# Kernel optimization log

Measured on AMD Instinct MI355X. Metric: run time of the kernel, lower is better.

## Reference

```python
import jax, jax.numpy as jnp
import numpy as np

DIM = 1024
HEADS = 16
HEAD_DIM = DIM // HEADS
D_FF = 4 * DIM
EPS = 1e-5


def _layernorm(x, g, b):
    mu = jnp.mean(x, axis=-1, keepdims=True)
    var = jnp.mean(jnp.square(x - mu), axis=-1, keepdims=True)
    return (x - mu) * jax.lax.rsqrt(var + EPS) * g + b


def setup_inputs() -> dict:
    key = jax.random.key(0)
    ks = jax.random.split(key, 8)
    s = 0.02
    return {
        "x": jax.random.normal(ks[0], (2, 2048, DIM), dtype=jnp.float32),
        "Wqkv": jax.random.normal(ks[1], (DIM, 3 * DIM), dtype=jnp.float32) * s,
        "bqkv": jnp.zeros((3 * DIM,), dtype=jnp.float32),
        "Wout": jax.random.normal(ks[2], (DIM, DIM), dtype=jnp.float32) * s,
        "bout": jnp.zeros((DIM,), dtype=jnp.float32),
        "W1": jax.random.normal(ks[3], (DIM, D_FF), dtype=jnp.float32) * s,
        "b1": jnp.zeros((D_FF,), dtype=jnp.float32),
        "W2": jax.random.normal(ks[4], (D_FF, DIM), dtype=jnp.float32) * s,
        "b2": jnp.zeros((DIM,), dtype=jnp.float32),
        "g1": jnp.ones((DIM,), dtype=jnp.float32),
        "be1": jnp.zeros((DIM,), dtype=jnp.float32),
        "g2": jnp.ones((DIM,), dtype=jnp.float32),
        "be2": jnp.zeros((DIM,), dtype=jnp.float32),
    }


def reference(x, Wqkv, bqkv, Wout, bout, W1, b1, W2, b2, g1, be1, g2, be2):
    B, T, C = x.shape
    # --- multi-head self-attention (explicit QK^T softmax, no mask/cache) ---
    qkv = (x @ Wqkv + bqkv).reshape(B, T, 3, HEADS, HEAD_DIM)
    q = qkv[:, :, 0].transpose(0, 2, 1, 3)  # (B,H,T,hd)
    k = qkv[:, :, 1].transpose(0, 2, 1, 3)
    v = qkv[:, :, 2].transpose(0, 2, 1, 3)
    scale = HEAD_DIM ** -0.5
    scores = jnp.einsum("bhqd,bhkd->bhqk", q, k) * scale  # (B,H,T,T)
    attn = jax.nn.softmax(scores, axis=-1)
    o = jnp.einsum("bhqk,bhkd->bhqd", attn, v)
    o = o.transpose(0, 2, 1, 3).reshape(B, T, C)
    attn_out = o @ Wout + bout
    # --- Post-LN: LN applied to sublayer output, then residual ---
    x = x + _layernorm(attn_out, g1, be1)
    # --- FFN with exact GELU ---
    h = jax.nn.gelu(x @ W1 + b1, approximate=False)
    ffn_out = h @ W2 + b2
    x = x + _layernorm(ffn_out, g2, be2)
    return x
```

## Files before the change

### kernel.cpp

```cpp
#include <hip/hip_runtime.h>
#include <cstdint>
#include <cstddef>

#define DIM 1024
#define HEADS 16
#define HD 64
#define DFF 4096
#define TSEQ 2048
#define EPS 1e-5f

#define WAITCNT_VM4 0xF74
#define WAITCNT_VM0 0xF70
#define WAITCNT_VM8 0xF78
#define WAITCNT_LGKM0 0xC07F

typedef __bf16 bf16x8 __attribute__((ext_vector_type(8)));
typedef __bf16 bf16x4 __attribute__((ext_vector_type(4)));
typedef float floatx4 __attribute__((ext_vector_type(4)));

__device__ __forceinline__ unsigned short f2bf(float f) {
  union { float f; unsigned int u; } v; v.f = f;
  return (unsigned short)((v.u + 0x7FFFu + ((v.u >> 16) & 1u)) >> 16);
}

__device__ __forceinline__ float exp2_fast(float x) {
#if __has_builtin(__builtin_amdgcn_exp2f)
  return __builtin_amdgcn_exp2f(x);
#else
  float r;
  asm("v_exp_f32 %0, %1" : "=v"(r) : "v"(x));
  return r;
#endif
}

__device__ __forceinline__ float gelu_f(float v) {
  const float u = v * (0.7978845608f + 0.0356774081f * v * v);
  const float e = __expf(2.0f * u);
  const float t = 1.0f - 2.0f / (e + 1.0f);
  return 0.5f * v * (1.0f + t);
}

__device__ __forceinline__ void async16(const void* g, void* l) {
  __builtin_amdgcn_global_load_lds(
      (const __attribute__((address_space(1))) void*)g,
      (__attribute__((address_space(3))) void*)l, 16, 0, 0);
}

__global__ __launch_bounds__(256) void prep_all(const float* __restrict__ x,
                                                const float* __restrict__ Wqkv,
                                                const float* __restrict__ Wout,
                                                const float* __restrict__ W1,
                                                const float* __restrict__ W2,
                                                unsigned short* __restrict__ xb,
                                                unsigned short* __restrict__ WqkvT,
                                                unsigned short* __restrict__ WoutT,
                                                unsigned short* __restrict__ W1T,
                                                unsigned short* __restrict__ W2T) {
  const int bid = blockIdx.x;
  const int tid = threadIdx.x;
  if (bid < 4096) {
    const int i = bid * 256 + tid;
    float4 v = ((const float4*)x)[i];
    ushort4 o;
    o.x = f2bf(v.x); o.y = f2bf(v.y); o.z = f2bf(v.z); o.w = f2bf(v.w);
    ((ushort4*)xb)[i] = o;
    return;
  }
  int id = bid - 4096;
  const float* src; unsigned short* dst; int R, C, gx;
  if (id < 3072)      {            src = Wqkv; dst = WqkvT; R = 1024; C = 3072; gx = 96; }
  else if (id < 4096) { id -= 3072; src = Wout; dst = WoutT; R = 1024; C = 1024; gx = 32; }
  else if (id < 8192) { id -= 4096; src = W1;   dst = W1T;   R = 1024; C = 4096; gx = 128; }
  else                { id -= 8192; src = W2;   dst = W2T;   R = 4096; C = 1024; gx = 32; }
  const int c0 = (id % gx) * 32, r0 = (id / gx) * 32;
  const int tx = tid & 31, ty = tid >> 5;
  __shared__ float tile[32][33];
#pragma unroll
  for (int i = 0; i < 32; i += 8)
    tile[ty + i][tx] = src[(size_t)(r0 + ty + i) * C + c0 + tx];
  __syncthreads();
#pragma unroll
  for (int i = 0; i < 32; i += 8)
    dst[(size_t)(c0 + ty + i) * R + r0 + tx] = f2bf(tile[tx][ty + i]);
}

#define GEMM256_CORE(APTR, BPTR, KT, KOFF, NG_)                                       \
  const int lane = tid & 63, wv = tid >> 6;                                           \
  const int l16 = lane & 15, quad = lane >> 4;                                        \
  const int wr = wv >> 2, wc = wv & 3;                                                \
  const int srow = tid >> 3;                                                          \
  const int scc = (tid & 7) ^ (srow & 7);                                             \
  const unsigned short* Asrc = (APTR) + (size_t)(bm + srow) * (KT) + (KOFF) + scc * 8;\
  const unsigned short* Bsrc = (BPTR) + (size_t)(bn + srow) * (KT) + (KOFF) + scc * 8;\
  auto stageKstep = [&](int buf, int kk) {                                            \
    char* dA = smem + buf * 65536;                                                    \
    char* dB = dA + 32768;                                                            \
    _Pragma("unroll")                                                                 \
    for (int h = 0; h < 2; h++)                                                       \
      _Pragma("unroll")                                                               \
      for (int j = 0; j < 2; j++) {                                                   \
        async16(Asrc + (size_t)(h * 128 + 64 * j) * (KT) + kk,                        \
                dA + h * 16384 + (j * 512 + tid) * 16);                               \
        async16(Bsrc + (size_t)(h * 128 + 64 * j) * (KT) + kk,                        \
                dB + h * 16384 + (j * 512 + tid) * 16);                               \
      }                                                                               \
  };                                                                                  \
  floatx4 acc[8][4] = {};                                                             \
  stageKstep(0, 0);                                                                   \
  __builtin_amdgcn_s_waitcnt(WAITCNT_VM0);                                            \
  __builtin_amdgcn_s_barrier();                                                       \
  for (int g = 0; g < (NG_); g++) {                                                   \
    const int p = g & 1;                                                              \
    const char* Ab = smem + p * 65536 + wr * 16384;                                   \
    const char* Bb = smem + p * 65536 + 32768 + (wc >> 1) * 16384;                    \
    bf16x8 bg[4][2];                                                                  \
    _Pragma("unroll")                                                                 \
    for (int q = 0; q < 4; q++) {                                                     \
      if (q == 0) {                                                                   \
        if (g + 1 < (NG_)) stageKstep(p ^ 1, (g + 1) << 6);                           \
        _Pragma("unroll")                                                             \
        for (int ni = 0; ni < 4; ni++) {                                              \
          const int lr = (wc & 1) * 64 + ni * 16 + l16;                               \
          _Pragma("unroll")                                                           \
          for (int ks = 0; ks < 2; ks++)                                              \
            bg[ni][ks] = *(const bf16x8*)(Bb + lr * 128 +                             \
                                          (((quad + 4 * ks) ^ (lr & 7)) * 16));       \
        }                                                                             \
      }                                                                               \
      bf16x8 af[2][2];                                                                \
      _Pragma("unroll")                                                               \
      for (int m = 0; m < 2; m++) {                                                   \
        const int lr = (q * 2 + m) * 16 + l16;                                        \
        _Pragma("unroll")                                                             \
        for (int ks = 0; ks < 2; ks++)                                                \
          af[m][ks] = *(const bf16x8*)(Ab + lr * 128 +                                \
                                       (((quad + 4 * ks) ^ (lr & 7)) * 16));          \
      }                                                                               \
      __builtin_amdgcn_s_barrier();                                                   \
      __builtin_amdgcn_s_waitcnt(WAITCNT_LGKM0);                                      \
      __builtin_amdgcn_s_setprio(1);                                                  \
      _Pragma("unroll")                                                               \
      for (int ks = 0; ks < 2; ks++)                                                  \
        _Pragma("unroll")                                                             \
        for (int ni = 0; ni < 4; ni++)                                                \
          _Pragma("unroll")                                                           \
          for (int m = 0; m < 2; m++)                                                 \
            acc[q * 2 + m][ni] = __builtin_amdgcn_mfma_f32_16x16x32_bf16(             \
                af[m][ks], bg[ni][ks], acc[q * 2 + m][ni], 0, 0, 0);                  \
      __builtin_amdgcn_s_setprio(0);                                                  \
      if (q == 3) __builtin_amdgcn_s_waitcnt(WAITCNT_VM0);                            \
      __builtin_amdgcn_s_barrier();                                                   \
    }                                                                                 \
  }

__global__ __launch_bounds__(512, 2) void gemm256g(const unsigned short* __restrict__ A,
                                                   const unsigned short* __restrict__ Bt,
                                                   const float* __restrict__ bias,
                                                   unsigned short* __restrict__ Cout,
                                                   int M, int N, int K) {
  extern __shared__ char smem[];
  const int tid = threadIdx.x;
  int bxx = blockIdx.x, byy = blockIdx.y;
  {
    const int id = byy * 16 + bxx;
    const int xcd = id & 7, sub = id >> 3;
    bxx = (xcd & 3) * 4 + (sub & 3);
    byy = (xcd >> 2) * 8 + (sub >> 2);
  }
  const int bm = byy * 256, bn = bxx * 256;
  GEMM256_CORE(A, Bt, K, 0, K >> 6)

  __syncthreads();
  unsigned short* eb = (unsigned short*)smem + wv * 1152;
  float bvv[4];
#pragma unroll
  for (int ni = 0; ni < 4; ni++) bvv[ni] = bias[bn + wc * 64 + ni * 16 + l16];
  const int lrow = lane >> 2, ck = lane & 3;
#pragma unroll
  for (int mi = 0; mi < 8; mi++) {
#pragma unroll
    for (int ni = 0; ni < 4; ni++)
#pragma unroll
      for (int r = 0; r < 4; r++)
        eb[(quad * 4 + r) * 72 + ni * 16 + l16] =
            f2bf(gelu_f(acc[mi][ni][r] + bvv[ni]));
    __syncthreads();
    unsigned short* gp =
        Cout + (size_t)(bm + wr * 128 + mi * 16 + lrow) * N + bn + wc * 64;
#pragma unroll
    for (int j = 0; j < 2; j++)
      *(uint4*)(gp + j * 32 + ck * 8) = *(const uint4*)&eb[lrow * 72 + j * 32 + ck * 8];
    __syncthreads();
  }
}

__global__ __launch_bounds__(512, 2) void gemm256_qkv(const unsigned short* __restrict__ A,
                                                      const unsigned short* __restrict__ Bt,
                                                      const float* __restrict__ bias,
                                                      unsigned short* __restrict__ Qg,
                                                      unsigned short* __restrict__ Kg,
                                                      unsigned short* __restrict__ Vtg) {
  extern __shared__ char smem[];
  const int tid = threadIdx.x;
  const int id = blockIdx.y * 12 + blockIdx.x;
  const int xcd = id / 24, sub = id % 24;
  const int bxx = (xcd & 3) * 3 + sub % 3;
  const int byy = (xcd >> 2) * 8 + sub / 3;
  const int bm = byy * 256, bn = bxx * 256;
  GEMM256_CORE(A, Bt, 1024, 0, 16)

  const float QSCALE = 0.125f * 1.44269504089f;
#pragma unroll
  for (int ni = 0; ni < 4; ni++) {
    const int col = bn + wc * 64 + ni * 16 + l16;
    const float bv = bias[col];
    const int sec = col >> 10;
    const int cc = col & 1023;
    const int hh = cc >> 6, dd = cc & 63;
#pragma unroll
    for (int mi = 0; mi < 8; mi++) {
      const int row0 = bm + wr * 128 + mi * 16 + quad * 4;
      const int b2 = row0 >> 11, tt0 = row0 & 2047;
      if (sec == 0) {
        unsigned short* q = Qg + ((size_t)(b2 * HEADS + hh) * TSEQ + tt0) * HD + dd;
#pragma unroll
        for (int r = 0; r < 4; r++)
          q[(size_t)r * HD] = f2bf((acc[mi][ni][r] + bv) * QSCALE);
      } else if (sec == 1) {
        unsigned short* k = Kg + ((size_t)(b2 * HEADS + hh) * TSEQ + tt0) * HD + dd;
#pragma unroll
        for (int r = 0; r < 4; r++)
          k[(size_t)r * HD] = f2bf(acc[mi][ni][r] + bv);
      } else {
        ushort4 o;
        o.x = f2bf(acc[mi][ni][0] + bv);
        o.y = f2bf(acc[mi][ni][1] + bv);
        o.z = f2bf(acc[mi][ni][2] + bv);
        o.w = f2bf(acc[mi][ni][3] + bv);
        *(ushort4*)(Vtg + ((size_t)(b2 * HEADS + hh) * HD + dd) * TSEQ + tt0) = o;
      }
    }
  }
}

__global__ __launch_bounds__(512, 2) void gemm256_sk(const unsigned short* __restrict__ A,
                                                     const unsigned short* __restrict__ Bt,
                                                     float* __restrict__ Cp,
                                                     int M, int N, int Ktot, int Ksl) {
  extern __shared__ char smem[];
  const int tid = threadIdx.x;
  const int id = (blockIdx.z * 16 + blockIdx.y) * 4 + blockIdx.x;
  const int xcd = id >> 5, sub = id & 31;
  const int bxx = sub & 3;
  const int u = xcd * 8 + (sub >> 2);
  const int byy = u & 15, bz = u >> 4;
  const int bm = byy * 256, bn = bxx * 256;
  const int koff = bz * Ksl;
  GEMM256_CORE(A, Bt, Ktot, koff, Ksl >> 6)

  float* out = Cp + (size_t)bz * M * (size_t)N;
#pragma unroll
  for (int ni = 0; ni < 4; ni++) {
    const int col = bn + wc * 64 + ni * 16 + l16;
#pragma unroll
    for (int mi = 0; mi < 8; mi++) {
      const int row0 = bm + wr * 128 + mi * 16 + quad * 4;
#pragma unroll
      for (int r = 0; r < 4; r++)
        out[(size_t)(row0 + r) * N + col] = acc[mi][ni][r];
    }
  }
}

__global__ __launch_bounds__(256, 4) void attn_mfma(const unsigned short* __restrict__ Qg,
                                                    const unsigned short* __restrict__ Kg,
                                                    const unsigned short* __restrict__ Vtg,
                                                    unsigned short* __restrict__ ob) {
  __shared__ __align__(16) char smem[40960];
  unsigned short* QPs = (unsigned short*)smem;

  const int bid = blockIdx.x;
  const int lid = (bid & 7) * 128 + (bid >> 3);
  const int qt = lid & 31;
  const int h = (lid >> 5) & 15;
  const int b = lid >> 9;
  const int tid = threadIdx.x;
  const int w = tid >> 6, lane = tid & 63, l16 = lane & 15, quad = lane >> 4;
  const int qg = w >> 1;
  const int kh = w & 1;

  const int r0 = tid >> 3;
  const int c0 = (tid & 7) ^ (r0 & 7);

  const char* Qbase = (const char*)(Qg + ((size_t)(b * HEADS + h) * TSEQ + qt * 64) * HD);
  const char* Kbase = (const char*)(Kg + (size_t)(b * HEADS + h) * TSEQ * HD);
  const char* Vbase = (const char*)(Vtg + (size_t)(b * HEADS + h) * HD * TSEQ);

  auto Ksp = [&](int s) -> char* { return smem + 8192 + s * 8192; };
  auto Vsp = [&](int s) -> char* { return smem + 24576 + s * 8192; };

  auto issueKV = [&](int s, int ch) {
    const size_t koff = (size_t)ch * 64;
#pragma unroll
    for (int i = 0; i < 2; i++) {
      async16(Kbase + (koff + r0 + i * 32) * 128 + c0 * 16, Ksp(s) + (i * 256 + tid) * 16);
      async16(Vbase + (size_t)(r0 + i * 32) * (TSEQ * 2) + koff * 2 + c0 * 16,
              Vsp(s) + (i * 256 + tid) * 16);
    }
  };

#pragma unroll
  for (int i = 0; i < 2; i++)
    async16(Qbase + (size_t)(r0 + i * 32) * 128 + c0 * 16, (char*)QPs + (i * 256 + tid) * 16);
  issueKV(0, 0);
  issueKV(1, 1);

  __builtin_amdgcn_s_waitcnt(WAITCNT_VM8);
  __builtin_amdgcn_s_barrier();

  bf16x8 qf[2][2];
#pragma unroll
  for (int mi = 0; mi < 2; mi++)
#pragma unroll
    for (int kt = 0; kt < 2; kt++) {
      const int row = qg * 32 + mi * 16 + l16;
      qf[mi][kt] = *(const bf16x8*)((const char*)QPs + row * 128 +
                                    (((quad + 4 * kt) ^ (row & 7)) * 16));
    }
  __builtin_amdgcn_s_waitcnt(WAITCNT_LGKM0);
  __builtin_amdgcn_sched_barrier(0);

  union { unsigned short u[8]; bf16x8 b; } onesu;
#pragma unroll
  for (int j = 0; j < 8; j++) onesu.u[j] = 0x3F80;
  const bf16x8 ones = onesu.b;

  floatx4 oacc[2][5] = {};
  char* Pw = (char*)QPs + w * 1152;

  const int NC = TSEQ / 64;
  int sidx = 0;
  for (int ch = 0; ch < NC; ch++) {
    if (ch < NC - 1) __builtin_amdgcn_s_waitcnt(WAITCNT_VM4);
    else             __builtin_amdgcn_s_waitcnt(WAITCNT_VM0);
    __builtin_amdgcn_s_barrier();

    floatx4 sacc[2][2] = {};
    __builtin_amdgcn_s_setprio(1);
#pragma unroll
    for (int kt = 0; kt < 2; kt++) {
#pragma unroll
      for (int ni = 0; ni < 2; ni++) {
        const int krow = kh * 32 + ni * 16 + l16;
        bf16x8 kf = *(const bf16x8*)(Ksp(sidx) + krow * 128 +
                                     (((quad + 4 * kt) ^ (krow & 7)) * 16));
#pragma unroll
        for (int mi = 0; mi < 2; mi++)
          sacc[mi][ni] =
              __builtin_amdgcn_mfma_f32_16x16x32_bf16(qf[mi][kt], kf, sacc[mi][ni], 0, 0, 0);
      }
    }
    __builtin_amdgcn_s_setprio(0);

    bf16x8 pf[2];
#pragma unroll
    for (int mi = 0; mi < 2; mi++) {
#pragma unroll
      for (int ni = 0; ni < 2; ni++)
#pragma unroll
        for (int r = 0; r < 4; r++) {
          const float p = exp2_fast(sacc[mi][ni][r]);
          const unsigned int pu = __builtin_bit_cast(unsigned int, p);
          *((unsigned short*)(Pw + (quad * 4 + r) * 72 + (ni * 16 + l16) * 2)) =
              (unsigned short)(pu >> 16);
        }
      union { bf16x8 v8; bf16x4 v4[2]; } u;
      u.v4[0] = *(const bf16x4*)(Pw + l16 * 72 + quad * 16);
      u.v4[1] = *(const bf16x4*)(Pw + l16 * 72 + quad * 16 + 8);
      pf[mi] = u.v8;
    }

    __builtin_amdgcn_s_setprio(1);
#pragma unroll
    for (int nj = 0; nj < 4; nj++) {
      const int vrow = nj * 16 + l16;
      bf16x8 vf = *(const bf16x8*)(Vsp(sidx) + vrow * 128 +
                                   (((quad + 4 * kh) ^ (vrow & 7)) * 16));
#pragma unroll
      for (int mi = 0; mi < 2; mi++)
        oacc[mi][nj] = __builtin_amdgcn_mfma_f32_16x16x32_bf16(pf[mi], vf, oacc[mi][nj], 0, 0, 0);
    }
#pragma unroll
    for (int mi = 0; mi < 2; mi++)
      oacc[mi][4] = __builtin_amdgcn_mfma_f32_16x16x32_bf16(pf[mi], ones, oacc[mi][4], 0, 0, 0);
    __builtin_amdgcn_s_setprio(0);

    __builtin_amdgcn_s_waitcnt(WAITCNT_LGKM0);
    __builtin_amdgcn_s_barrier();
    if (ch + 2 < NC) issueKV(sidx, ch + 2);
    sidx ^= 1;
  }

  __syncthreads();
  float* Op = (float*)smem + qg * (32 * 66);
  if (kh == 1) {
#pragma unroll
    for (int mi = 0; mi < 2; mi++)
#pragma unroll
      for (int r = 0; r < 4; r++) {
        const int row = mi * 16 + quad * 4 + r;
#pragma unroll
        for (int nj = 0; nj < 4; nj++)
          Op[row * 66 + nj * 16 + l16] = oacc[mi][nj][r];
        if (l16 == 0) Op[row * 66 + 64] = oacc[mi][4][r];
      }
  }
  __syncthreads();
  if (kh == 0) {
#pragma unroll
    for (int mi = 0; mi < 2; mi++)
#pragma unroll
      for (int r = 0; r < 4; r++) {
        const int row = mi * 16 + quad * 4 + r;
        const float inv = 1.0f / (oacc[mi][4][r] + Op[row * 66 + 64]);
        const int t = qt * 64 + qg * 32 + row;
        unsigned short* orow = ob + (size_t)(b * TSEQ + t) * DIM + h * HD + l16;
#pragma unroll
        for (int nj = 0; nj < 4; nj++)
          orow[nj * 16] = f2bf((oacc[mi][nj][r] + Op[row * 66 + nj * 16 + l16]) * inv);
      }
  }
}

template <int NP, int WBF>
__global__ __launch_bounds__(256) void add_ln_red(const float* __restrict__ xin,
                                                  const float* __restrict__ parts,
                                                  const float* __restrict__ bias,
                                                  const float* __restrict__ gw,
                                                  const float* __restrict__ bw,
                                                  float* __restrict__ xout,
                                                  unsigned short* __restrict__ xbf) {
  const size_t MN = (size_t)4096 * DIM;
  const int row = blockIdx.x;
  const int tid = threadIdx.x;
  const int c = tid * 4;
  const size_t base = (size_t)row * DIM;
  float4 v = *(const float4*)(parts + base + c);
#pragma unroll
  for (int p = 1; p < NP; p++) {
    float4 t = *(const float4*)(parts + p * MN + base + c);
    v.x += t.x; v.y += t.y; v.z += t.z; v.w += t.w;
  }
  float4 bb = *(const float4*)(bias + c);
  v.x += bb.x; v.y += bb.y; v.z += bb.z; v.w += bb.w;

  float s = v.x + v.y + v.z + v.w;
  float s2 = v.x * v.x + v.y * v.y + v.z * v.z + v.w * v.w;
#pragma unroll
  for (int off = 1; off < 64; off <<= 1) {
    s += __shfl_xor(s, off);
    s2 += __shfl_xor(s2, off);
  }
  __shared__ float rsum[4], rsq[4];
  if ((tid & 63) == 0) { rsum[tid >> 6] = s; rsq[tid >> 6] = s2; }
  __syncthreads();
  s = rsum[0] + rsum[1] + rsum[2] + rsum[3];
  s2 = rsq[0] + rsq[1] + rsq[2] + rsq[3];
  const float mu = s * (1.0f / DIM);
  const float var = s2 * (1.0f / DIM) - mu * mu;
  const float rstd = rsqrtf(var + EPS);
  float4 xv = *(const float4*)(xin + base + c);
  float4 gv = *(const float4*)(gw + c);
  float4 bv = *(const float4*)(bw + c);
  float4 o;
  o.x = xv.x + (v.x - mu) * rstd * gv.x + bv.x;
  o.y = xv.y + (v.y - mu) * rstd * gv.y + bv.y;
  o.z = xv.z + (v.z - mu) * rstd * gv.z + bv.z;
  o.w = xv.w + (v.w - mu) * rstd * gv.w + bv.w;
  *(float4*)(xout + base + c) = o;
  if (WBF) {
    ushort4 ob;
    ob.x = f2bf(o.x); ob.y = f2bf(o.y); ob.z = f2bf(o.z); ob.w = f2bf(o.w);
    *(ushort4*)(xbf + base + c) = ob;
  }
}

extern "C" void kernel_launch(void* const* d_in, const int* in_sizes, int n_in,
                              void* d_out, int out_size, void* d_ws, size_t ws_size,
                              hipStream_t stream) {
  const float* x    = (const float*)d_in[0];
  const float* Wqkv = (const float*)d_in[1];
  const float* bqkv = (const float*)d_in[2];
  const float* Wout = (const float*)d_in[3];
  const float* bout = (const float*)d_in[4];
  const float* W1   = (const float*)d_in[5];
  const float* b1   = (const float*)d_in[6];
  const float* W2   = (const float*)d_in[7];
  const float* b2   = (const float*)d_in[8];
  const float* g1   = (const float*)d_in[9];
  const float* be1  = (const float*)d_in[10];
  const float* g2   = (const float*)d_in[11];
  const float* be2  = (const float*)d_in[12];

  static bool s_attr = false;
  if (!s_attr) {
    hipFuncSetAttribute((const void*)gemm256g,
                        hipFuncAttributeMaxDynamicSharedMemorySize, 131072);
    hipFuncSetAttribute((const void*)gemm256_qkv,
                        hipFuncAttributeMaxDynamicSharedMemorySize, 131072);
    hipFuncSetAttribute((const void*)gemm256_sk,
                        hipFuncAttributeMaxDynamicSharedMemorySize, 131072);
    s_attr = true;
  }

  char* w = (char*)d_ws;
  const size_t MB = 1048576;
  unsigned short* xb     = (unsigned short*)(w + 0 * MB);
  unsigned short* WqkvT  = (unsigned short*)(w + 8 * MB);
  unsigned short* WoutT  = (unsigned short*)(w + 14 * MB);
  unsigned short* W1T    = (unsigned short*)(w + 16 * MB);
  unsigned short* W2T    = (unsigned short*)(w + 24 * MB);
  unsigned short* Qb     = (unsigned short*)(w + 32 * MB);
  unsigned short* Kb     = (unsigned short*)(w + 40 * MB);
  unsigned short* Vtb    = (unsigned short*)(w + 48 * MB);
  unsigned short* obuf   = (unsigned short*)(w + 64 * MB);
  float*          atno_p = (float*)(w + 72 * MB);
  float*          x1     = (float*)(w + 136 * MB);
  unsigned short* x1b    = (unsigned short*)(w + 152 * MB);
  unsigned short* hb     = (unsigned short*)(w + 32 * MB);
  float*          ffn_p  = (float*)(w + 72 * MB);

  prep_all<<<16384, 256, 0, stream>>>(x, Wqkv, Wout, W1, W2, xb, WqkvT, WoutT, W1T, W2T);

  gemm256_qkv<<<dim3(12, 16), 512, 131072, stream>>>(xb, WqkvT, bqkv, Qb, Kb, Vtb);
  attn_mfma<<<1024, 256, 0, stream>>>(Qb, Kb, Vtb, obuf);
  gemm256_sk<<<dim3(4, 16, 4), 512, 131072, stream>>>(obuf, WoutT, atno_p, 4096, 1024, 1024, 256);
  add_ln_red<4, 1><<<4096, 256, 0, stream>>>(x, atno_p, bout, g1, be1, x1, x1b);
  gemm256g<<<dim3(16, 16), 512, 131072, stream>>>(x1b, W1T, b1, hb, 4096, 4096, 1024);
  gemm256_sk<<<dim3(4, 16, 4), 512, 131072, stream>>>(hb, W2T, ffn_p, 4096, 1024, 4096, 1024);
  add_ln_red<4, 0><<<4096, 256, 0, stream>>>(x1, ffn_p, b2, g2, be2, (float*)d_out, nullptr);
}
```

Baseline: 362.7 us.

## Replace 256-tile split-K GEMM with 128-tile triple-buffered kernel and split-K of two

```diff
diff --git a/kernel.cpp b/kernel.cpp
--- a/kernel.cpp
+++ b/kernel.cpp
@@ -83,6 +83,40 @@
   for (int i = 0; i < 32; i += 8)
     dst[(size_t)(c0 + ty + i) * R + r0 + tx] = f2bf(tile[tx][ty + i]);
 }
+
+#define PIPELINED_KLOOP3(NIT)                                                        \
+  auto issue = [&](int s, int k0) {                                                  \
+    async16(Ab0 + k0, &lds[s][tid * 8]);                                             \
+    async16(Ab1 + k0, &lds[s][2048 + tid * 8]);                                      \
+    async16(Bb0 + k0, &lds[s][4096 + tid * 8]);                                      \
+    async16(Bb1 + k0, &lds[s][6144 + tid * 8]);                                      \
+  };                                                                                 \
+  issue(0, 0);                                                                       \
+  issue(1, 32);                                                                      \
+  int sidx = 0;                                                                      \
+  for (int k = 0; k < (NIT); k++) {                                                  \
+    if (k < (NIT)-1) __builtin_amdgcn_s_waitcnt(WAITCNT_VM4);                        \
+    else             __builtin_amdgcn_s_waitcnt(WAITCNT_VM0);                        \
+    __builtin_amdgcn_s_barrier();                                                    \
+    if (k + 2 < (NIT)) {                                                             \
+      int s2 = sidx + 2; if (s2 >= 3) s2 -= 3;                                       \
+      issue(s2, (k + 2) * 32);                                                       \
+    }                                                                                \
+    bf16x8 af[4], bg[4];                                                             \
+    _Pragma("unroll")                                                                \
+    for (int mi = 0; mi < 4; mi++)                                                   \
+      af[mi] = *(const bf16x8*)&lds[sidx][(wm + mi * 16 + l16) * 32 + quad * 8];     \
+    _Pragma("unroll")                                                                \
+    for (int ni = 0; ni < 4; ni++)                                                   \
+      bg[ni] = *(const bf16x8*)&lds[sidx][4096 + (wn + ni * 16 + l16) * 32 + quad * 8]; \
+    _Pragma("unroll")                                                                \
+    for (int mi = 0; mi < 4; mi++)                                                   \
+      _Pragma("unroll")                                                              \
+      for (int ni = 0; ni < 4; ni++)                                                 \
+        acc[mi][ni] =                                                                \
+            __builtin_amdgcn_mfma_f32_16x16x32_bf16(af[mi], bg[ni], acc[mi][ni], 0, 0, 0); \
+    sidx = (sidx == 2) ? 0 : sidx + 1;                                               \
+  }
 
 #define GEMM256_CORE(APTR, BPTR, KT, KOFF, NG_)                                       \
   const int lane = tid & 63, wv = tid >> 6;                                           \
@@ -243,28 +277,43 @@
   }
 }
 
-__global__ __launch_bounds__(512, 2) void gemm256_sk(const unsigned short* __restrict__ A,
-                                                     const unsigned short* __restrict__ Bt,
-                                                     float* __restrict__ Cp,
-                                                     int M, int N, int Ktot, int Ksl) {
-  extern __shared__ char smem[];
+__global__ __launch_bounds__(256) void gemm_splitk(const unsigned short* __restrict__ A,
+                                                   const unsigned short* __restrict__ Bt,
+                                                   float* __restrict__ Cp,
+                                                   int M, int N, int Ktot, int Ksl) {
+  __shared__ unsigned short lds[3][8192];
   const int tid = threadIdx.x;
-  const int id = (blockIdx.z * 16 + blockIdx.y) * 4 + blockIdx.x;
-  const int xcd = id >> 5, sub = id & 31;
-  const int bxx = sub & 3;
-  const int u = xcd * 8 + (sub >> 2);
-  const int byy = u & 15, bz = u >> 4;
-  const int bm = byy * 256, bn = bxx * 256;
+  const int id = (blockIdx.z * 32 + blockIdx.y) * 8 + blockIdx.x;
+  const int xcd = id & 7, sub = id >> 3;
+  const int bxx = sub & 7;
+  const int byz = xcd * (gridDim.z * 4) + (sub >> 3);
+  const int byy = byz & 31, bz = byz >> 5;
+  const int bm = byy * 128, bn = bxx * 128;
   const int koff = bz * Ksl;
-  GEMM256_CORE(A, Bt, Ktot, koff, Ksl >> 6)
+  const int wave = tid >> 6, lane = tid & 63;
+  const int l16 = lane & 15, quad = lane >> 4;
+  const int wm = (wave >> 1) * 64, wn = (wave & 1) * 64;
+
+  floatx4 acc[4][4] = {};
+
+  const int srow = tid >> 2;
+  const int scol = (tid & 3) * 8;
+
+  const unsigned short* Ab0 = A + (size_t)(bm + srow) * Ktot + koff + scol;
+  const unsigned short* Ab1 = A + (size_t)(bm + 64 + srow) * Ktot + koff + scol;
+  const unsigned short* Bb0 = Bt + (size_t)(bn + srow) * Ktot + koff + scol;
+  const unsigned short* Bb1 = Bt + (size_t)(bn + 64 + srow) * Ktot + koff + scol;
+
+  const int nit = Ksl >> 5;
+  PIPELINED_KLOOP3(nit)
 
   float* out = Cp + (size_t)bz * M * (size_t)N;
 #pragma unroll
   for (int ni = 0; ni < 4; ni++) {
-    const int col = bn + wc * 64 + ni * 16 + l16;
-#pragma unroll
-    for (int mi = 0; mi < 8; mi++) {
-      const int row0 = bm + wr * 128 + mi * 16 + quad * 4;
+    const int col = bn + wn + ni * 16 + l16;
+#pragma unroll
+    for (int mi = 0; mi < 4; mi++) {
+      const int row0 = bm + wm + mi * 16 + quad * 4;
 #pragma unroll
       for (int r = 0; r < 4; r++)
         out[(size_t)(row0 + r) * N + col] = acc[mi][ni][r];
@@ -508,8 +557,6 @@
                         hipFuncAttributeMaxDynamicSharedMemorySize, 131072);
     hipFuncSetAttribute((const void*)gemm256_qkv,
                         hipFuncAttributeMaxDynamicSharedMemorySize, 131072);
-    hipFuncSetAttribute((const void*)gemm256_sk,
-                        hipFuncAttributeMaxDynamicSharedMemorySize, 131072);
     s_attr = true;
   }
 
@@ -525,18 +572,18 @@
   unsigned short* Vtb    = (unsigned short*)(w + 48 * MB);
   unsigned short* obuf   = (unsigned short*)(w + 64 * MB);
   float*          atno_p = (float*)(w + 72 * MB);
-  float*          x1     = (float*)(w + 136 * MB);
-  unsigned short* x1b    = (unsigned short*)(w + 152 * MB);
-  unsigned short* hb     = (unsigned short*)(w + 32 * MB);
-  float*          ffn_p  = (float*)(w + 72 * MB);
+  float*          x1     = (float*)(w + 104 * MB);
+  unsigned short* x1b    = (unsigned short*)(w + 120 * MB);
+  unsigned short* hb     = (unsigned short*)(w + 128 * MB);
+  float*          ffn_p  = (float*)(w + 32 * MB);
 
   prep_all<<<16384, 256, 0, stream>>>(x, Wqkv, Wout, W1, W2, xb, WqkvT, WoutT, W1T, W2T);
 
   gemm256_qkv<<<dim3(12, 16), 512, 131072, stream>>>(xb, WqkvT, bqkv, Qb, Kb, Vtb);
   attn_mfma<<<1024, 256, 0, stream>>>(Qb, Kb, Vtb, obuf);
-  gemm256_sk<<<dim3(4, 16, 4), 512, 131072, stream>>>(obuf, WoutT, atno_p, 4096, 1024, 1024, 256);
-  add_ln_red<4, 1><<<4096, 256, 0, stream>>>(x, atno_p, bout, g1, be1, x1, x1b);
+  gemm_splitk<<<dim3(8, 32, 2), 256, 0, stream>>>(obuf, WoutT, atno_p, 4096, 1024, 1024, 512);
+  add_ln_red<2, 1><<<4096, 256, 0, stream>>>(x, atno_p, bout, g1, be1, x1, x1b);
   gemm256g<<<dim3(16, 16), 512, 131072, stream>>>(x1b, W1T, b1, hb, 4096, 4096, 1024);
-  gemm256_sk<<<dim3(4, 16, 4), 512, 131072, stream>>>(hb, W2T, ffn_p, 4096, 1024, 4096, 1024);
-  add_ln_red<4, 0><<<4096, 256, 0, stream>>>(x1, ffn_p, b2, g2, be2, (float*)d_out, nullptr);
-}
+  gemm_splitk<<<dim3(8, 32, 2), 256, 0, stream>>>(hb, W2T, ffn_p, 4096, 1024, 4096, 2048);
+  add_ln_red<2, 0><<<4096, 256, 0, stream>>>(x1, ffn_p, b2, g2, be2, (float*)d_out, nullptr);
+}
```

New measurement: 345.2 us. -4.8%, faster.
